# Kernel tuning notes

Hardware: AMD Instinct MI355X
Metric: run time of the kernel (lower is better)

## Reference

```python
import jax, jax.numpy as jnp
import numpy as np

HIDDEN_DIM = 2048
NUM_HEADS = 16
HEAD_DIM = HIDDEN_DIM // NUM_HEADS


def setup_inputs() -> dict:
    key = jax.random.key(0)
    ks = jax.random.split(key, 5)
    B, S, D = 2, 2048, HIDDEN_DIM
    scale = 1.0 / np.sqrt(D)
    return {
        "x": jax.random.normal(ks[0], (B, S, D), dtype=jnp.float32),
        "w_q": jax.random.normal(ks[1], (D, D), dtype=jnp.float32) * scale,
        "w_k": jax.random.normal(ks[2], (D, D), dtype=jnp.float32) * scale,
        "w_v": jax.random.normal(ks[3], (D, D), dtype=jnp.float32) * scale,
        "w_o": jax.random.normal(ks[4], (D, D), dtype=jnp.float32) * scale,
        "causal": 1,
    }


def _attention(q, k, v, causal):
    # q,k,v: (B, S, D) -> split heads -> (B, H, S, d)
    B, S, D = q.shape
    q = q.reshape(B, S, NUM_HEADS, HEAD_DIM).transpose(0, 2, 1, 3)
    k = k.reshape(B, S, NUM_HEADS, HEAD_DIM).transpose(0, 2, 1, 3)
    v = v.reshape(B, S, NUM_HEADS, HEAD_DIM).transpose(0, 2, 1, 3)
    scale = 1.0 / np.sqrt(HEAD_DIM)
    # scores: (B, H, S, S)
    s = jnp.einsum("bhqd,bhkd->bhqk", q, k) * scale
    if causal:
        qpos = jnp.arange(S)[:, None]
        kpos = jnp.arange(S)[None, :]
        s = jnp.where(kpos > qpos, -jnp.inf, s)
    # stable softmax; rows that are fully -inf cannot occur with causal mask
    p = jax.nn.softmax(s, axis=-1)
    o = jnp.einsum("bhqk,bhkd->bhqd", p, v)
    return o.transpose(0, 2, 1, 3).reshape(B, S, D)


def reference(x, w_q, w_k, w_v, w_o, causal):
    q = x @ w_q.T
    k = x @ w_k.T
    v = x @ w_v.T
    o = _attention(q, k, v, bool(causal))
    return o @ w_o.T
```

## Files before the change

### kernel.cpp

```cpp
#include <hip/hip_runtime.h>


typedef __attribute__((ext_vector_type(8))) short short8;
typedef __attribute__((ext_vector_type(4))) short bfs4;
typedef __attribute__((ext_vector_type(4))) float floatx4;

__device__ __forceinline__ void gl_lds16(const void* g, void* l) {
  __builtin_amdgcn_global_load_lds((const __attribute__((address_space(1))) void*)g,
                                   (__attribute__((address_space(3))) void*)l, 16, 0, 0);
}

__device__ __forceinline__ short f2bf(float f) {
  union { float f; unsigned u; } a; a.f = f;
  unsigned r = a.u + 0x7FFFu + ((a.u >> 16) & 1u);
  return (short)(r >> 16);
}

__global__ __launch_bounds__(256) void cvt_bf16(
    const float* __restrict__ s0, const float* __restrict__ s1,
    const float* __restrict__ s2, const float* __restrict__ s3,
    const float* __restrict__ s4,
    short* __restrict__ d0, short* __restrict__ d1, short* __restrict__ d2,
    short* __restrict__ d3, short* __restrict__ d4,
    int n0, int nw) {
  const int z = blockIdx.z;
  const float* s = (z == 0) ? s0 : (z == 1) ? s1 : (z == 2) ? s2 : (z == 3) ? s3 : s4;
  short* d      = (z == 0) ? d0 : (z == 1) ? d1 : (z == 2) ? d2 : (z == 3) ? d3 : d4;
  const int n   = (z == 0) ? n0 : nw;
  const int stride = gridDim.x * blockDim.x * 4;
  for (int i = (blockIdx.x * blockDim.x + threadIdx.x) * 4; i < n; i += stride) {
    float4 v = *(const float4*)(s + i);
    bfs4 o;
    o[0] = f2bf(v.x); o[1] = f2bf(v.y); o[2] = f2bf(v.z); o[3] = f2bf(v.w);
    *(bfs4*)(d + i) = o;
  }
}

__global__ __launch_bounds__(256, 2) void gemm_bt(
    const short* __restrict__ A,
    const short* __restrict__ B0, const short* __restrict__ B1, const short* __restrict__ B2,
    short* __restrict__ C0, short* __restrict__ C1, short* __restrict__ C2,
    int M, int N, int K) {
  const short* Bm = (blockIdx.z == 0) ? B0 : ((blockIdx.z == 1) ? B1 : B2);
  short* C = (blockIdx.z == 0) ? C0 : ((blockIdx.z == 1) ? C1 : C2);

  __shared__ short As[128 * 64];
  __shared__ short Bs[128 * 64];

  const int tid = threadIdx.x;
  const int w = tid >> 6, l = tid & 63;
  const int lane15 = l & 15, quad = l >> 4;
  const int wr = w >> 1, wc = w & 1;
  const int row0 = blockIdx.y * 128;
  const int col0 = blockIdx.x * 128;

  floatx4 acc[4][4] = {};
  const int srow = l >> 3;
  const int sg = l & 7;

  for (int k0 = 0; k0 < K; k0 += 64) {
#pragma unroll
    for (int j = 0; j < 4; ++j) {
      int chunk = j * 4 + w;
      int row = chunk * 8 + srow;
      int g = sg ^ (row & 7);
      gl_lds16(A  + (size_t)(row0 + row) * K + k0 + g * 8, &As[chunk * 512]);
      gl_lds16(Bm + (size_t)(col0 + row) * K + k0 + g * 8, &Bs[chunk * 512]);
    }
    __syncthreads();
#pragma unroll
    for (int ks = 0; ks < 2; ++ks) {
      short8 af[4], bf[4];
#pragma unroll
      for (int i = 0; i < 4; ++i) {
        int rowA = wr * 64 + i * 16 + lane15;
        af[i] = *(const short8*)&As[rowA * 64 + (((ks * 4 + quad) ^ (rowA & 7)) << 3)];
        int rowB = wc * 64 + i * 16 + lane15;
        bf[i] = *(const short8*)&Bs[rowB * 64 + (((ks * 4 + quad) ^ (rowB & 7)) << 3)];
      }
#pragma unroll
      for (int i = 0; i < 4; ++i)
#pragma unroll
        for (int jj = 0; jj < 4; ++jj)
          acc[i][jj] = __builtin_amdgcn_mfma_f32_16x16x32_bf16(af[i], bf[jj], acc[i][jj], 0, 0, 0);
    }
    __syncthreads();
  }

#pragma unroll
  for (int i = 0; i < 4; ++i)
#pragma unroll
    for (int jj = 0; jj < 4; ++jj)
#pragma unroll
      for (int r = 0; r < 4; ++r) {
        int row = row0 + wr * 64 + i * 16 + quad * 4 + r;
        int col = col0 + wc * 64 + jj * 16 + lane15;
        C[(size_t)row * N + col] = f2bf(acc[i][jj][r]);
      }
}

__global__ __launch_bounds__(256, 2) void gemm_bt_f32out(
    const short* __restrict__ A, const short* __restrict__ Bm,
    float* __restrict__ C, int M, int N, int K) {
  __shared__ short As[128 * 64];
  __shared__ short Bs[128 * 64];

  const int tid = threadIdx.x;
  const int w = tid >> 6, l = tid & 63;
  const int lane15 = l & 15, quad = l >> 4;
  const int wr = w >> 1, wc = w & 1;
  const int row0 = blockIdx.y * 128;
  const int col0 = blockIdx.x * 128;

  floatx4 acc[4][4] = {};
  const int srow = l >> 3;
  const int sg = l & 7;

  for (int k0 = 0; k0 < K; k0 += 64) {
#pragma unroll
    for (int j = 0; j < 4; ++j) {
      int chunk = j * 4 + w;
      int row = chunk * 8 + srow;
      int g = sg ^ (row & 7);
      gl_lds16(A  + (size_t)(row0 + row) * K + k0 + g * 8, &As[chunk * 512]);
      gl_lds16(Bm + (size_t)(col0 + row) * K + k0 + g * 8, &Bs[chunk * 512]);
    }
    __syncthreads();
#pragma unroll
    for (int ks = 0; ks < 2; ++ks) {
      short8 af[4], bf[4];
#pragma unroll
      for (int i = 0; i < 4; ++i) {
        int rowA = wr * 64 + i * 16 + lane15;
        af[i] = *(const short8*)&As[rowA * 64 + (((ks * 4 + quad) ^ (rowA & 7)) << 3)];
        int rowB = wc * 64 + i * 16 + lane15;
        bf[i] = *(const short8*)&Bs[rowB * 64 + (((ks * 4 + quad) ^ (rowB & 7)) << 3)];
      }
#pragma unroll
      for (int i = 0; i < 4; ++i)
#pragma unroll
        for (int jj = 0; jj < 4; ++jj)
          acc[i][jj] = __builtin_amdgcn_mfma_f32_16x16x32_bf16(af[i], bf[jj], acc[i][jj], 0, 0, 0);
    }
    __syncthreads();
  }

#pragma unroll
  for (int i = 0; i < 4; ++i)
#pragma unroll
    for (int jj = 0; jj < 4; ++jj)
#pragma unroll
      for (int r = 0; r < 4; ++r) {
        int row = row0 + wr * 64 + i * 16 + quad * 4 + r;
        int col = col0 + wc * 64 + jj * 16 + lane15;
        C[(size_t)row * N + col] = acc[i][jj][r];
      }
}

__global__ __launch_bounds__(512, 4) void attn_fused(
    const short* __restrict__ Qg, const short* __restrict__ Kg,
    const short* __restrict__ Vg, short* __restrict__ Og,
    const int* __restrict__ causal_p) {
  constexpr int S = 2048, D = 2048, HDim = 128;
  constexpr int PS = 40;
  __shared__ __align__(16) short smem[21760];
  short* Qs  = smem;
  short* Ks0 = smem;
  short* Ks1 = smem + 4096;
  short* Vt0 = smem + 8192;
  short* Vt1 = smem + 12288;
  short* Ps  = smem + 16384;
  float* aLds = (float*)(smem + 21504);
  floatx4* F4 = (floatx4*)smem;

  const int tid = threadIdx.x;
  const int w = tid >> 6, l = tid & 63;
  const int lane15 = l & 15, quad = l >> 4;
  const int w4 = w & 3, grp = w >> 2;
  const int bh = blockIdx.y, b = bh >> 4, h = bh & 15;
  const size_t rbase = (size_t)b * S;
  const int c0 = h * HDim;
  const int causal = *causal_p;
  short* Pw = Ps + w * (16 * PS);
  constexpr float SCL = 0.08838834764831845f * 1.4426950408889634f;

  const int vt8 = tid & 255, vtile = tid >> 8;
  const int vs = vt8 & 31, vdg = vt8 >> 5;
  const int sg8 = vs >> 3, so = vs & 7;
  short* Vtb = vtile ? Vt1 : Vt0;

#pragma unroll 1
  for (int ph = 0; ph < 2; ++ph) {
    const int jt = ph ? (31 - blockIdx.x) : blockIdx.x;
    const int q0 = jt * 64;
    const int wrow0 = q0 + w4 * 16;

#pragma unroll
    for (int j = 0; j < 2; ++j) {
      int row = j * 32 + w * 4 + quad;
      int gs = lane15 ^ (row & 7);
      gl_lds16(Qg + (rbase + q0 + row) * D + c0 + gs * 8, &Qs[(j * 8 + w) * 512]);
    }
    __syncthreads();
    short8 qf[4];
#pragma unroll
    for (int ks = 0; ks < 4; ++ks) {
      int row = w4 * 16 + lane15;
      qf[ks] = *(const short8*)&Qs[row * HDim + (((ks * 4 + quad) ^ (row & 7)) << 3)];
    }
    __syncthreads();

    floatx4 ot[8] = {};
    float psum[4] = {0.f, 0.f, 0.f, 0.f};
    const int ktiles = causal ? (q0 / 32 + 2) : (S / 32);
    const int iters = ktiles >> 1;

    for (int it = 0; it < iters; ++it) {
      const int k0A = it * 64;
      {
        int row = w * 4 + quad;
        int gs = lane15 ^ (row & 7);
        gl_lds16(Kg + (rbase + k0A + row) * D + c0 + gs * 8, &Ks0[w * 512]);
        gl_lds16(Kg + (rbase + k0A + 32 + row) * D + c0 + gs * 8, &Ks1[w * 512]);
      }
      {
        const short* vp = Vg + (rbase + k0A + vtile * 32 + vs) * D + c0 + vdg * 16;
        short8 v0 = *(const short8*)vp;
        short8 v1 = *(const short8*)(vp + 8);
#pragma unroll
        for (int e = 0; e < 8; ++e) {
          int d0 = vdg * 16 + e, d1 = vdg * 16 + 8 + e;
          Vtb[d0 * 32 + ((sg8 ^ (d0 & 3)) << 3) + so] = v0[e];
          Vtb[d1 * 32 + ((sg8 ^ (d1 & 3)) << 3) + so] = v1[e];
        }
      }
      __syncthreads();

      const int k0 = k0A + grp * 32;
      const short* Kc = grp ? Ks1 : Ks0;
      const short* Vc = grp ? Vt1 : Vt0;
      if (!causal || k0 <= wrow0 + 15) {
        floatx4 sacc[2] = {};
#pragma unroll
        for (int ks = 0; ks < 4; ++ks) {
          short8 kf0, kf1;
          {
            int row = lane15;
            kf0 = *(const short8*)&Kc[row * HDim + (((ks * 4 + quad) ^ (row & 7)) << 3)];
            row = 16 + lane15;
            kf1 = *(const short8*)&Kc[row * HDim + (((ks * 4 + quad) ^ (row & 7)) << 3)];
          }
          sacc[0] = __builtin_amdgcn_mfma_f32_16x16x32_bf16(qf[ks], kf0, sacc[0], 0, 0, 0);
          sacc[1] = __builtin_amdgcn_mfma_f32_16x16x32_bf16(qf[ks], kf1, sacc[1], 0, 0, 0);
        }
#pragma unroll
        for (int r = 0; r < 4; ++r) {
          int prow = quad * 4 + r;
          int qrow = wrow0 + prow;
          float s0 = fminf(sacc[0][r] * SCL, 115.0f);
          float s1 = fminf(sacc[1][r] * SCL, 115.0f);
          float p0 = exp2f(s0);
          float p1 = exp2f(s1);
          if (causal) {
            if (k0 + lane15 > qrow)      p0 = 0.f;
            if (k0 + 16 + lane15 > qrow) p1 = 0.f;
          }
          psum[r] += p0 + p1;
          Pw[prow * PS + lane15]      = f2bf(p0);
          Pw[prow * PS + 16 + lane15] = f2bf(p1);
        }
        short8 pfr = *(const short8*)&Pw[lane15 * PS + quad * 8];
#pragma unroll
        for (int cd = 0; cd < 8; ++cd) {
          int d = cd * 16 + lane15;
          short8 vf = *(const short8*)&Vc[d * 32 + ((quad ^ (d & 3)) << 3)];
          ot[cd] = __builtin_amdgcn_mfma_f32_16x16x32_bf16(vf, pfr, ot[cd], 0, 0, 0);
        }
      }
      __syncthreads();
    }

#pragma unroll
    for (int r = 0; r < 4; ++r) {
      float s = psum[r];
      s += __shfl_xor(s, 1, 64);
      s += __shfl_xor(s, 2, 64);
      s += __shfl_xor(s, 4, 64);
      s += __shfl_xor(s, 8, 64);
      if (lane15 == 0) aLds[grp * 64 + w4 * 16 + quad * 4 + r] = s;
    }
    if (grp == 1) {
      int qrow = w4 * 16 + lane15;
#pragma unroll
      for (int cd = 0; cd < 8; ++cd)
        F4[qrow * 32 + ((cd * 4 + quad) ^ ((qrow & 7) << 2))] = ot[cd];
    }
    __syncthreads();
    float invq = 0.f;
    if (grp == 0) {
      int qrow = w4 * 16 + lane15;
      invq = 1.0f / (aLds[qrow] + aLds[64 + qrow]);
#pragma unroll
      for (int cd = 0; cd < 8; ++cd) {
        floatx4 o2 = F4[qrow * 32 + ((cd * 4 + quad) ^ ((qrow & 7) << 2))];
        ot[cd] += o2;
      }
    }
    __syncthreads();
    if (grp == 0) {
      int qrow = w4 * 16 + lane15;
#pragma unroll
      for (int cd = 0; cd < 8; ++cd)
#pragma unroll
        for (int r = 0; r < 4; ++r) {
          int col = cd * 16 + quad * 4 + r;
          Qs[qrow * HDim + (((col >> 3) ^ (qrow & 7)) << 3) + (col & 7)] =
              f2bf(ot[cd][r] * invq);
        }
    }
    __syncthreads();
#pragma unroll
    for (int i = 0; i < 2; ++i) {
      int c = i * 512 + tid;
      int row = c >> 4, g = c & 15;
      *(short8*)(Og + (rbase + q0 + row) * D + c0 + g * 8) =
          *(const short8*)&Qs[row * HDim + ((g ^ (row & 7)) << 3)];
    }
    __syncthreads();
  }
}

extern "C" void kernel_launch(void* const* d_in, const int* in_sizes, int n_in,
                              void* d_out, int out_size, void* d_ws, size_t ws_size,
                              hipStream_t stream) {
  const float* x  = (const float*)d_in[0];
  const float* wq = (const float*)d_in[1];
  const float* wk = (const float*)d_in[2];
  const float* wv = (const float*)d_in[3];
  const float* wo = (const float*)d_in[4];
  const int* causal = (const int*)d_in[5];
  float* out = (float*)d_out;

  const int M = 4096, N = 2048, K = 2048;
  const int NX = M * K;
  const int NW = N * K;

  char* ws = (char*)d_ws;
  short* xb  = (short*)(ws);
  short* wqb = (short*)(ws + 16u * 1024 * 1024);
  short* wkb = (short*)(ws + 24u * 1024 * 1024);
  short* wvb = (short*)(ws + 32u * 1024 * 1024);
  short* wob = (short*)(ws + 40u * 1024 * 1024);
  short* q   = (short*)(ws + 48u * 1024 * 1024);
  short* k   = (short*)(ws + 64u * 1024 * 1024);
  short* v   = (short*)(ws + 80u * 1024 * 1024);
  short* o   = (short*)(ws + 96u * 1024 * 1024);

  dim3 blk(256);
  cvt_bf16<<<dim3(2048, 1, 5), blk, 0, stream>>>(x, wq, wk, wv, wo,
                                                 xb, wqb, wkb, wvb, wob, NX, NW);
  gemm_bt<<<dim3(N / 128, M / 128, 3), blk, 0, stream>>>(xb, wqb, wkb, wvb,
                                                         q, k, v, M, N, K);
  attn_fused<<<dim3(16, 32), dim3(512), 0, stream>>>(q, k, v, o, causal);
  gemm_bt_f32out<<<dim3(N / 128, M / 128, 1), blk, 0, stream>>>(o, wob, out, M, N, K);
}
```

Before: 396.7 us.

## Double-buffer K/V tiles in fused attention to prefetch the next tile

Each block now holds two K/V buffers in shared memory. While the current tile is being computed, it issues the async K copy to LDS and the global V loads for the next tile. The prefetched V values are transposed into the spare buffer after compute, which leaves one barrier per iteration instead of two. The aim is to hide global memory latency behind the MFMA work, at the cost of nearly doubling LDS per block, which may reduce how many blocks fit on a CU.

```diff
diff --git a/kernel.cpp b/kernel.cpp
--- a/kernel.cpp
+++ b/kernel.cpp
@@ -163,14 +163,10 @@
     const int* __restrict__ causal_p) {
   constexpr int S = 2048, D = 2048, HDim = 128;
   constexpr int PS = 40;
-  __shared__ __align__(16) short smem[21760];
+  __shared__ __align__(16) short smem[38144];
+  short* Ps  = smem + 32768;
+  float* aLds = (float*)(smem + 37888);
   short* Qs  = smem;
-  short* Ks0 = smem;
-  short* Ks1 = smem + 4096;
-  short* Vt0 = smem + 8192;
-  short* Vt1 = smem + 12288;
-  short* Ps  = smem + 16384;
-  float* aLds = (float*)(smem + 21504);
   floatx4* F4 = (floatx4*)smem;
 
   const int tid = threadIdx.x;
@@ -187,7 +183,9 @@
   const int vt8 = tid & 255, vtile = tid >> 8;
   const int vs = vt8 & 31, vdg = vt8 >> 5;
   const int sg8 = vs >> 3, so = vs & 7;
-  short* Vtb = vtile ? Vt1 : Vt0;
+
+  const int krow = w * 4 + quad;
+  const int kgs = lane15 ^ (krow & 7);
 
 #pragma unroll 1
   for (int ph = 0; ph < 2; ++ph) {
@@ -215,30 +213,43 @@
     const int ktiles = causal ? (q0 / 32 + 2) : (S / 32);
     const int iters = ktiles >> 1;
 
+    short* Kcur = smem;
+    short* Knxt = smem + 8192;
+    short* Vcur = smem + 16384;
+    short* Vnxt = smem + 24576;
+
+    gl_lds16(Kg + (rbase + krow) * D + c0 + kgs * 8, &Kcur[w * 512]);
+    gl_lds16(Kg + (rbase + 32 + krow) * D + c0 + kgs * 8, &Kcur[4096 + w * 512]);
+    {
+      const short* vp = Vg + (rbase + vtile * 32 + vs) * D + c0 + vdg * 16;
+      short8 v0 = *(const short8*)vp;
+      short8 v1 = *(const short8*)(vp + 8);
+      short* Vtb = Vcur + vtile * 4096;
+#pragma unroll
+      for (int e = 0; e < 8; ++e) {
+        int d0 = vdg * 16 + e, d1 = vdg * 16 + 8 + e;
+        Vtb[d0 * 32 + ((sg8 ^ (d0 & 3)) << 3) + so] = v0[e];
+        Vtb[d1 * 32 + ((sg8 ^ (d1 & 3)) << 3) + so] = v1[e];
+      }
+    }
+    __syncthreads();
+
     for (int it = 0; it < iters; ++it) {
       const int k0A = it * 64;
-      {
-        int row = w * 4 + quad;
-        int gs = lane15 ^ (row & 7);
-        gl_lds16(Kg + (rbase + k0A + row) * D + c0 + gs * 8, &Ks0[w * 512]);
-        gl_lds16(Kg + (rbase + k0A + 32 + row) * D + c0 + gs * 8, &Ks1[w * 512]);
-      }
-      {
-        const short* vp = Vg + (rbase + k0A + vtile * 32 + vs) * D + c0 + vdg * 16;
-        short8 v0 = *(const short8*)vp;
-        short8 v1 = *(const short8*)(vp + 8);
-#pragma unroll
-        for (int e = 0; e < 8; ++e) {
-          int d0 = vdg * 16 + e, d1 = vdg * 16 + 8 + e;
-          Vtb[d0 * 32 + ((sg8 ^ (d0 & 3)) << 3) + so] = v0[e];
-          Vtb[d1 * 32 + ((sg8 ^ (d1 & 3)) << 3) + so] = v1[e];
-        }
-      }
-      __syncthreads();
+      const bool pf = (it + 1 < iters);
+      short8 pv0, pv1;
+      if (pf) {
+        const int k0N = k0A + 64;
+        gl_lds16(Kg + (rbase + k0N + krow) * D + c0 + kgs * 8, &Knxt[w * 512]);
+        gl_lds16(Kg + (rbase + k0N + 32 + krow) * D + c0 + kgs * 8, &Knxt[4096 + w * 512]);
+        const short* vp = Vg + (rbase + k0N + vtile * 32 + vs) * D + c0 + vdg * 16;
+        pv0 = *(const short8*)vp;
+        pv1 = *(const short8*)(vp + 8);
+      }
 
       const int k0 = k0A + grp * 32;
-      const short* Kc = grp ? Ks1 : Ks0;
-      const short* Vc = grp ? Vt1 : Vt0;
+      const short* Kc = Kcur + grp * 4096;
+      const short* Vc = Vcur + grp * 4096;
       if (!causal || k0 <= wrow0 + 15) {
         floatx4 sacc[2] = {};
 #pragma unroll
@@ -277,7 +288,19 @@
           ot[cd] = __builtin_amdgcn_mfma_f32_16x16x32_bf16(vf, pfr, ot[cd], 0, 0, 0);
         }
       }
+
+      if (pf) {
+        short* Vtb = Vnxt + vtile * 4096;
+#pragma unroll
+        for (int e = 0; e < 8; ++e) {
+          int d0 = vdg * 16 + e, d1 = vdg * 16 + 8 + e;
+          Vtb[d0 * 32 + ((sg8 ^ (d0 & 3)) << 3) + so] = pv0[e];
+          Vtb[d1 * 32 + ((sg8 ^ (d1 & 3)) << 3) + so] = pv1[e];
+        }
+      }
       __syncthreads();
+      short* t = Kcur; Kcur = Knxt; Knxt = t;
+      t = Vcur; Vcur = Vnxt; Vnxt = t;
     }
 
 #pragma unroll
```

Result: no change. 389.1 us (-1.9%).
